# Kernel optimization log

Measured on AMD Instinct MI355X. Metric: run time of the kernel, lower is better.

Reference implementation:

```python
import jax, jax.numpy as jnp
import numpy as np

B, S, D, H = 2, 2048, 768, 12
HD = D // H
WINDOW = 64  # local_attention // 2
ROPE_THETA = 10000.0
NEG = -1e9


def setup_inputs() -> dict:
    key = jax.random.key(0)
    k1, k2, k3 = jax.random.split(key, 3)
    hidden_states = jax.random.normal(k1, (B, S, D), dtype=jnp.float32)
    Wqkv_w = jax.random.normal(k2, (3 * D, D), dtype=jnp.float32) * (D ** -0.5)
    Wo_w = jax.random.normal(k3, (D, D), dtype=jnp.float32) * (D ** -0.5)
    position_ids = jnp.broadcast_to(jnp.arange(S, dtype=jnp.int64 if jax.config.jax_enable_x64 else jnp.int32), (B, S))
    # additive sliding-window mask: 0 inside window, -1e9 outside (matches torch ModernBert mask construction)
    idx = np.arange(S)
    dist = np.abs(idx[:, None] - idx[None, :])
    sliding_window_mask = jnp.asarray(np.where(dist <= WINDOW, 0.0, NEG), dtype=jnp.float32)[None, None]  # [1,1,S,S]
    return {"hidden_states": hidden_states, "Wqkv_w": Wqkv_w, "Wo_w": Wo_w,
            "sliding_window_mask": sliding_window_mask, "position_ids": position_ids}


def _rotate_half(x):
    x1, x2 = jnp.split(x, 2, axis=-1)
    return jnp.concatenate([-x2, x1], axis=-1)


def reference(hidden_states, Wqkv_w, Wo_w, sliding_window_mask, position_ids):
    b, s, d = hidden_states.shape
    qkv = hidden_states @ Wqkv_w.T                      # [B,S,3D]
    qkv = qkv.reshape(b, s, 3, H, HD)
    q = qkv[:, :, 0].transpose(0, 2, 1, 3)              # [B,H,S,HD]
    k = qkv[:, :, 1].transpose(0, 2, 1, 3)
    v = qkv[:, :, 2].transpose(0, 2, 1, 3)
    # RoPE
    inv_freq = 1.0 / (ROPE_THETA ** (jnp.arange(0, HD, 2, dtype=jnp.float32) / HD))  # [HD/2]
    freqs = position_ids.astype(jnp.float32)[..., None] * inv_freq                   # [B,S,HD/2]
    emb = jnp.concatenate([freqs, freqs], axis=-1)                                   # [B,S,HD]
    cos = jnp.cos(emb)[:, None]                          # [B,1,S,HD]
    sin = jnp.sin(emb)[:, None]
    q = q * cos + _rotate_half(q) * sin
    k = k * cos + _rotate_half(k) * sin
    scale = HD ** -0.5
    scores = jnp.einsum('bhqd,bhkd->bhqk', q, k) * scale + sliding_window_mask       # [B,H,S,S]
    attn = jax.nn.softmax(scores.astype(jnp.float32), axis=-1).astype(q.dtype)
    out = jnp.einsum('bhqk,bhkd->bhqd', attn, v)         # [B,H,S,HD]
    out = out.transpose(0, 2, 1, 3).reshape(b, s, d)     # [B,S,D]
    return out @ Wo_w.T
```

## Files before the change

### kernel.cpp

```cpp
#include <hip/hip_runtime.h>
#include <hip/hip_bf16.h>
#include <cmath>

#define B_   2
#define S_   2048
#define D_   768
#define H_   12
#define HD_  64
#define WIN_ 64

typedef __bf16 bf16x8 __attribute__((ext_vector_type(8)));
typedef __bf16 bf16x4 __attribute__((ext_vector_type(4)));
typedef float  f32x4  __attribute__((ext_vector_type(4)));
typedef unsigned int u32;

__device__ __forceinline__ void async_ld16(const void* g, void* l) {
    __builtin_amdgcn_global_load_lds(
        (__attribute__((address_space(1))) void*)(size_t)g,
        (__attribute__((address_space(3))) void*)(u32)(size_t)l,
        16, 0, 0);
}

#define WAIT_VM0   0x0F70
#define WAIT_VM8   0x0F78
#define WAIT_LGKM0 0xC07F

#define NHS (B_ * S_ * D_)
#define NWQ (3 * D_ * D_)
#define NWO (D_ * D_)

__global__ __launch_bounds__(256) void to_bf16_3(const float* __restrict__ a,
                                                 const float* __restrict__ b,
                                                 const float* __restrict__ c,
                                                 __bf16* __restrict__ oa,
                                                 __bf16* __restrict__ ob,
                                                 __bf16* __restrict__ oc) {
    const int NA = NHS / 4, NB = NWQ / 4;
    int v = blockIdx.x * 256 + threadIdx.x;
    const float* src; __bf16* dst; int idx;
    if (v < NA)           { src = a; dst = oa; idx = v; }
    else if (v < NA + NB) { src = b; dst = ob; idx = v - NA; }
    else                  { src = c; dst = oc; idx = v - NA - NB; }
    float4 x = ((const float4*)src)[idx];
    bf16x4 y = { (__bf16)x.x, (__bf16)x.y, (__bf16)x.z, (__bf16)x.w };
    *(bf16x4*)(dst + (size_t)idx * 4) = y;
}

template <int MODE>
__global__ __launch_bounds__(128) void gemm_w(const __bf16* __restrict__ A,
                                              const __bf16* __restrict__ Bw,
                                              float* __restrict__ C,
                                              __bf16* __restrict__ qkv,
                                              __bf16* __restrict__ vt,
                                              const int* __restrict__ pos,
                                              int M, int N, int K) {
    __shared__ __attribute__((aligned(16))) char smem[2 * 16384];

    const int tid  = threadIdx.x;
    const int w    = tid >> 6;
    const int lane = tid & 63;
    const int id = blockIdx.x;
    const int m0 = (id & 63) << 6;
    const int n0 = (((id >> 6) << 1) + w) << 6;
    const int fr = lane & 15, fq = lane >> 4;
    const int sw = (fq + (fr >> 1)) & 3;

    __bf16* St = (__bf16*)(smem + w * 16384);

    f32x4 acc[4][4] = {};

    const int nkw = K >> 5;

    auto issue = [&](int ki, int buf) {
        const int k0 = ki << 5;
        __bf16* As = St + buf * 4096;
        __bf16* Bs = As + 2048;
        #pragma unroll
        for (int i = 0; i < 4; ++i) {
            const int c = i * 64 + lane;
            const int row = c >> 2, ccp = c & 3;
            const int cc = (ccp - (row >> 1)) & 3;
            async_ld16(A  + (size_t)(m0 + row) * K + k0 + cc * 8, As + c * 8);
            async_ld16(Bw + (size_t)(n0 + row) * K + k0 + cc * 8, Bs + c * 8);
        }
    };

    issue(0, 0);

    for (int ki = 0; ki < nkw; ++ki) {
        const int buf = ki & 1;
        if (ki + 1 < nkw) {
            __builtin_amdgcn_s_waitcnt(WAIT_LGKM0);
            issue(ki + 1, buf ^ 1);
            __builtin_amdgcn_s_waitcnt(WAIT_VM8);
        } else {
            __builtin_amdgcn_s_waitcnt(WAIT_VM0);
        }

        __bf16* As = St + buf * 4096;
        __bf16* Bs = As + 2048;
        bf16x8 af[4], bfv[4];
        #pragma unroll
        for (int t = 0; t < 4; ++t) {
            af[t]  = *(const bf16x8*)(As + (t * 16 + fr) * 32 + sw * 8);
            bfv[t] = *(const bf16x8*)(Bs + (t * 16 + fr) * 32 + sw * 8);
        }
        #pragma unroll
        for (int ti = 0; ti < 4; ++ti)
            #pragma unroll
            for (int tj = 0; tj < 4; ++tj)
                acc[ti][tj] = __builtin_amdgcn_mfma_f32_16x16x32_bf16(
                    af[ti], bfv[tj], acc[ti][tj], 0, 0, 0);
    }

    __builtin_amdgcn_s_waitcnt(WAIT_LGKM0);

    if (MODE == 0) {
        float* eL = (float*)St;
        #pragma unroll
        for (int half = 0; half < 2; ++half) {
            #pragma unroll
            for (int ti = 0; ti < 2; ++ti)
                #pragma unroll
                for (int tj = 0; tj < 4; ++tj)
                    #pragma unroll
                    for (int r = 0; r < 4; ++r)
                        eL[(ti * 16 + fq * 4 + r) * 65 + tj * 16 + fr] =
                            acc[half * 2 + ti][tj][r];
            #pragma unroll
            for (int p = 0; p < 8; ++p) {
                const int rc = p * 4 + (lane >> 4), ch = lane & 15;
                f32x4 vv = *(const f32x4*)(eL + rc * 65 + ch * 4);
                *(f32x4*)(C + (size_t)(m0 + half * 32 + rc) * N + n0 + ch * 4) = vv;
            }
        }
    } else if (n0 < 2 * D_) {
        const float invf0 = __powf(10000.0f, -(float)fr * (1.0f / 32.0f));
        const float invf1 = __powf(10000.0f, -(float)(16 + fr) * (1.0f / 32.0f));
        #pragma unroll
        for (int ti = 0; ti < 4; ++ti)
            #pragma unroll
            for (int r = 0; r < 4; ++r) {
                const int row = m0 + ti * 16 + fq * 4 + r;
                const float p = (float)pos[row];
                float s0, c0, s1, c1;
                __sincosf(p * invf0, &s0, &c0);
                __sincosf(p * invf1, &s1, &c1);
                const float x0 = acc[ti][0][r], x1 = acc[ti][2][r];
                acc[ti][0][r] = x0 * c0 - x1 * s0;
                acc[ti][2][r] = x1 * c0 + x0 * s0;
                const float y0 = acc[ti][1][r], y1 = acc[ti][3][r];
                acc[ti][1][r] = y0 * c1 - y1 * s1;
                acc[ti][3][r] = y1 * c1 + y0 * s1;
            }
        __bf16* eL = (__bf16*)St;
        #pragma unroll
        for (int ti = 0; ti < 4; ++ti)
            #pragma unroll
            for (int tj = 0; tj < 4; ++tj)
                #pragma unroll
                for (int r = 0; r < 4; ++r)
                    eL[(ti * 16 + fq * 4 + r) * 68 + tj * 16 + fr] = (__bf16)acc[ti][tj][r];
        #pragma unroll
        for (int p = 0; p < 8; ++p) {
            const int rq = p * 8 + (lane >> 3), ch = lane & 7;
            bf16x8 vv = *(const bf16x8*)(eL + rq * 68 + ch * 8);
            *(bf16x8*)(qkv + (size_t)(m0 + rq) * (2 * D_) + n0 + ch * 8) = vv;
        }
    } else {
        const int h = (n0 - 2 * D_) >> 6;
        const int bb = m0 >> 11, t0 = m0 & (S_ - 1);
        __bf16* eL = (__bf16*)St;
        #pragma unroll
        for (int ti = 0; ti < 4; ++ti)
            #pragma unroll
            for (int tj = 0; tj < 4; ++tj)
                #pragma unroll
                for (int r = 0; r < 4; ++r)
                    eL[(tj * 16 + fr) * 68 + ti * 16 + fq * 4 + r] = (__bf16)acc[ti][tj][r];
        const size_t vb = (size_t)((bb * H_ + h) * HD_) * S_ + t0;
        #pragma unroll
        for (int p = 0; p < 8; ++p) {
            const int d = p * 8 + (lane >> 3), ch = lane & 7;
            bf16x8 vv = *(const bf16x8*)(eL + d * 68 + ch * 8);
            *(bf16x8*)(vt + vb + (size_t)d * S_ + ch * 8) = vv;
        }
    }
}

__global__ __launch_bounds__(256) void attn_mfma(const __bf16* __restrict__ qkv,
                                                 const __bf16* __restrict__ vt,
                                                 __bf16* __restrict__ outb) {
    __shared__ __attribute__((aligned(16))) __bf16 smem[24576];
    __bf16* Ks  = smem;
    __bf16* Vts = smem + 12288;

    const int i0  = blockIdx.x * 64;
    const int h   = blockIdx.y;
    const int b   = blockIdx.z;
    const int tid = threadIdx.x;
    const int w = tid >> 6, lane = tid & 63;
    const int fr = lane & 15, fq = lane >> 4;
    const int wq0 = w * 16;

    #pragma unroll
    for (int i = 0; i < 6; ++i) {
        int c = i * 256 + tid;
        int ks = (i >= 3);
        int rem = c - ks * 768;
        int cc = rem & 3, row = rem >> 2;
        int j = i0 - 64 + row; j = min(max(j, 0), S_ - 1);
        async_ld16(qkv + ((size_t)b * S_ + j) * (2 * D_) + D_ + h * HD_ + ks * 32 + cc * 8,
                   Ks + c * 8);
    }
    const size_t vbase = (size_t)((b * H_ + h) * HD_) * S_;
    #pragma unroll
    for (int i = 0; i < 6; ++i) {
        int c = i * 256 + tid;
        int ks = c >> 8, rem = c & 255, d = rem >> 2, cc = rem & 3;
        int key = i0 - 64 + ks * 32 + cc * 8;
        key = min(max(key, 0), S_ - 8);
        async_ld16(vt + vbase + (size_t)d * S_ + key, Vts + c * 8);
    }

    const size_t qrow = ((size_t)b * S_ + i0 + wq0 + fr) * (2 * D_) + h * HD_;
    bf16x8 aq[2];
    aq[0] = *(const bf16x8*)(qkv + qrow + fq * 8);
    aq[1] = *(const bf16x8*)(qkv + qrow + 32 + fq * 8);

    __syncthreads();

    f32x4 sc[12] = {};
    #pragma unroll
    for (int nt = 0; nt < 12; ++nt) {
        #pragma unroll
        for (int ks = 0; ks < 2; ++ks) {
            bf16x8 bk = *(const bf16x8*)(Ks + (ks * 192 + nt * 16 + fr) * 32 + fq * 8);
            sc[nt] = __builtin_amdgcn_mfma_f32_16x16x32_bf16(aq[ks], bk, sc[nt], 0, 0, 0);
        }
    }

    float mx[4] = { -1e30f, -1e30f, -1e30f, -1e30f };
    #pragma unroll
    for (int nt = 0; nt < 12; ++nt) {
        const int jr = nt * 16 + fr;
        const int j  = i0 - 64 + jr;
        const bool jv = (j >= 0) && (j < S_);
        #pragma unroll
        for (int r = 0; r < 4; ++r) {
            const int ir = wq0 + fq * 4 + r + 64;
            const int dd = ir - jr;
            const bool v = jv && (dd <= WIN_) && (dd >= -WIN_);
            sc[nt][r] = v ? sc[nt][r] * 0.125f : -1e30f;
            mx[r] = fmaxf(mx[r], sc[nt][r]);
        }
    }
    #pragma unroll
    for (int r = 0; r < 4; ++r)
        #pragma unroll
        for (int off = 1; off < 16; off <<= 1)
            mx[r] = fmaxf(mx[r], __shfl_xor(mx[r], off, 64));

    float sm[4] = { 0.f, 0.f, 0.f, 0.f };
    #pragma unroll
    for (int nt = 0; nt < 12; ++nt)
        #pragma unroll
        for (int r = 0; r < 4; ++r) {
            float e = __expf(sc[nt][r] - mx[r]);
            sc[nt][r] = e;
            sm[r] += e;
        }
    #pragma unroll
    for (int r = 0; r < 4; ++r) {
        #pragma unroll
        for (int off = 1; off < 16; off <<= 1)
            sm[r] += __shfl_xor(sm[r], off, 64);
        sm[r] = 1.0f / sm[r];
    }

    __syncthreads();

    __bf16* Pw = Ks + w * 3072;
    #pragma unroll
    for (int nt = 0; nt < 12; ++nt) {
        const int ks = nt >> 1, kk = (nt & 1) * 16 + fr;
        #pragma unroll
        for (int r = 0; r < 4; ++r)
            Pw[(ks * 16 + fq * 4 + r) * 32 + kk] = (__bf16)(sc[nt][r] * sm[r]);
    }

    f32x4 oacc[4] = {};
    #pragma unroll
    for (int ks = 0; ks < 6; ++ks) {
        bf16x8 ap = *(const bf16x8*)(Pw + (ks * 16 + fr) * 32 + fq * 8);
        #pragma unroll
        for (int nt2 = 0; nt2 < 4; ++nt2) {
            bf16x8 bv = *(const bf16x8*)(Vts + (ks * 64 + nt2 * 16 + fr) * 32 + fq * 8);
            oacc[nt2] = __builtin_amdgcn_mfma_f32_16x16x32_bf16(ap, bv, oacc[nt2], 0, 0, 0);
        }
    }

    #pragma unroll
    for (int nt2 = 0; nt2 < 4; ++nt2)
        #pragma unroll
        for (int r = 0; r < 4; ++r)
            Pw[(fq * 4 + r) * 68 + nt2 * 16 + fr] = (__bf16)oacc[nt2][r];
    #pragma unroll
    for (int p = 0; p < 2; ++p) {
        const int q = p * 8 + (lane >> 3), ch = lane & 7;
        bf16x8 vv = *(const bf16x8*)(Pw + q * 68 + ch * 8);
        *(bf16x8*)(outb + ((size_t)b * S_ + i0 + wq0 + q) * D_ + h * HD_ + ch * 8) = vv;
    }
}

extern "C" void kernel_launch(void* const* d_in, const int* in_sizes, int n_in,
                              void* d_out, int out_size, void* d_ws, size_t ws_size,
                              hipStream_t stream) {
    const float* hs   = (const float*)d_in[0];
    const float* wqkv = (const float*)d_in[1];
    const float* wo   = (const float*)d_in[2];
    const int*   pos  = (const int*)d_in[4];
    float* out = (float*)d_out;

    __bf16* base    = (__bf16*)d_ws;
    __bf16* hs_bf   = base;
    __bf16* wqkv_bf = hs_bf + NHS;
    __bf16* wo_bf   = wqkv_bf + NWQ;
    __bf16* qkv     = wo_bf + NWO;
    __bf16* vt      = qkv + (size_t)(B_ * S_) * (2 * D_);
    __bf16* attn_bf = vt + (size_t)B_ * H_ * HD_ * S_;

    to_bf16_3<<<(NHS + NWQ + NWO) / 1024, 256, 0, stream>>>(
        hs, wqkv, wo, hs_bf, wqkv_bf, wo_bf);

    gemm_w<1><<<dim3(64 * (3 * D_ / 128)), 128, 0, stream>>>(
        hs_bf, wqkv_bf, nullptr, qkv, vt, pos, B_ * S_, 3 * D_, D_);

    attn_mfma<<<dim3(S_ / 64, H_, B_), 256, 0, stream>>>(qkv, vt, attn_bf);

    gemm_w<0><<<dim3(64 * (D_ / 128)), 128, 0, stream>>>(
        attn_bf, wo_bf, out, nullptr, nullptr, nullptr, B_ * S_, D_, D_);
}
```

Before: 146.9 us.

## Load GEMM fragments directly from global into registers with double buffering

Result: slower. 193.5 us (+31.8%).

```diff
diff --git a/kernel.cpp b/kernel.cpp
--- a/kernel.cpp
+++ b/kernel.cpp
@@ -20,10 +20,6 @@
         (__attribute__((address_space(3))) void*)(u32)(size_t)l,
         16, 0, 0);
 }
-
-#define WAIT_VM0   0x0F70
-#define WAIT_VM8   0x0F78
-#define WAIT_LGKM0 0xC07F
 
 #define NHS (B_ * S_ * D_)
 #define NWQ (3 * D_ * D_)
@@ -47,76 +43,61 @@
 }
 
 template <int MODE>
-__global__ __launch_bounds__(128) void gemm_w(const __bf16* __restrict__ A,
-                                              const __bf16* __restrict__ Bw,
-                                              float* __restrict__ C,
-                                              __bf16* __restrict__ qkv,
-                                              __bf16* __restrict__ vt,
-                                              const int* __restrict__ pos,
-                                              int M, int N, int K) {
-    __shared__ __attribute__((aligned(16))) char smem[2 * 16384];
+__global__ __launch_bounds__(256, 3) void gemm_r(const __bf16* __restrict__ A,
+                                                 const __bf16* __restrict__ Bw,
+                                                 float* __restrict__ C,
+                                                 __bf16* __restrict__ qkv,
+                                                 __bf16* __restrict__ vt,
+                                                 const int* __restrict__ pos,
+                                                 int M, int N, int K) {
+    __shared__ __attribute__((aligned(16))) char esmem[4][8704];
 
     const int tid  = threadIdx.x;
     const int w    = tid >> 6;
     const int lane = tid & 63;
     const int id = blockIdx.x;
     const int m0 = (id & 63) << 6;
-    const int n0 = (((id >> 6) << 1) + w) << 6;
+    const int n0 = (((id >> 6) << 2) + w) << 6;
     const int fr = lane & 15, fq = lane >> 4;
-    const int sw = (fq + (fr >> 1)) & 3;
-
-    __bf16* St = (__bf16*)(smem + w * 16384);
+
+    const __bf16* Ap = A  + (size_t)(m0 + fr) * K + fq * 8;
+    const __bf16* Bp = Bw + (size_t)(n0 + fr) * K + fq * 8;
+    const size_t rstep = (size_t)16 * K;
 
     f32x4 acc[4][4] = {};
-
-    const int nkw = K >> 5;
-
-    auto issue = [&](int ki, int buf) {
-        const int k0 = ki << 5;
-        __bf16* As = St + buf * 4096;
-        __bf16* Bs = As + 2048;
-        #pragma unroll
-        for (int i = 0; i < 4; ++i) {
-            const int c = i * 64 + lane;
-            const int row = c >> 2, ccp = c & 3;
-            const int cc = (ccp - (row >> 1)) & 3;
-            async_ld16(A  + (size_t)(m0 + row) * K + k0 + cc * 8, As + c * 8);
-            async_ld16(Bw + (size_t)(n0 + row) * K + k0 + cc * 8, Bs + c * 8);
+    bf16x8 a0[4], b0[4], a1[4], b1[4];
+
+    auto LD = [&](bf16x8 (&ar)[4], bf16x8 (&br)[4], int kk) {
+        const int ko = kk << 5;
+        #pragma unroll
+        for (int t = 0; t < 4; ++t) {
+            ar[t] = *(const bf16x8*)(Ap + (size_t)t * rstep + ko);
+            br[t] = *(const bf16x8*)(Bp + (size_t)t * rstep + ko);
         }
     };
-
-    issue(0, 0);
-
-    for (int ki = 0; ki < nkw; ++ki) {
-        const int buf = ki & 1;
-        if (ki + 1 < nkw) {
-            __builtin_amdgcn_s_waitcnt(WAIT_LGKM0);
-            issue(ki + 1, buf ^ 1);
-            __builtin_amdgcn_s_waitcnt(WAIT_VM8);
-        } else {
-            __builtin_amdgcn_s_waitcnt(WAIT_VM0);
-        }
-
-        __bf16* As = St + buf * 4096;
-        __bf16* Bs = As + 2048;
-        bf16x8 af[4], bfv[4];
-        #pragma unroll
-        for (int t = 0; t < 4; ++t) {
-            af[t]  = *(const bf16x8*)(As + (t * 16 + fr) * 32 + sw * 8);
-            bfv[t] = *(const bf16x8*)(Bs + (t * 16 + fr) * 32 + sw * 8);
-        }
+    auto MM = [&](const bf16x8 (&ar)[4], const bf16x8 (&br)[4]) {
         #pragma unroll
         for (int ti = 0; ti < 4; ++ti)
             #pragma unroll
             for (int tj = 0; tj < 4; ++tj)
                 acc[ti][tj] = __builtin_amdgcn_mfma_f32_16x16x32_bf16(
-                    af[ti], bfv[tj], acc[ti][tj], 0, 0, 0);
-    }
-
-    __builtin_amdgcn_s_waitcnt(WAIT_LGKM0);
+                    ar[ti], br[tj], acc[ti][tj], 0, 0, 0);
+    };
+
+    const int nkw = K >> 5;
+    LD(a0, b0, 0);
+    for (int kk = 0; kk + 2 < nkw; kk += 2) {
+        LD(a1, b1, kk + 1);
+        MM(a0, b0);
+        LD(a0, b0, kk + 2);
+        MM(a1, b1);
+    }
+    LD(a1, b1, nkw - 1);
+    MM(a0, b0);
+    MM(a1, b1);
 
     if (MODE == 0) {
-        float* eL = (float*)St;
+        float* eL = (float*)esmem[w];
         #pragma unroll
         for (int half = 0; half < 2; ++half) {
             #pragma unroll
@@ -153,7 +134,7 @@
                 acc[ti][1][r] = y0 * c1 - y1 * s1;
                 acc[ti][3][r] = y1 * c1 + y0 * s1;
             }
-        __bf16* eL = (__bf16*)St;
+        __bf16* eL = (__bf16*)esmem[w];
         #pragma unroll
         for (int ti = 0; ti < 4; ++ti)
             #pragma unroll
@@ -170,7 +151,7 @@
     } else {
         const int h = (n0 - 2 * D_) >> 6;
         const int bb = m0 >> 11, t0 = m0 & (S_ - 1);
-        __bf16* eL = (__bf16*)St;
+        __bf16* eL = (__bf16*)esmem[w];
         #pragma unroll
         for (int ti = 0; ti < 4; ++ti)
             #pragma unroll
@@ -333,11 +314,11 @@
     to_bf16_3<<<(NHS + NWQ + NWO) / 1024, 256, 0, stream>>>(
         hs, wqkv, wo, hs_bf, wqkv_bf, wo_bf);
 
-    gemm_w<1><<<dim3(64 * (3 * D_ / 128)), 128, 0, stream>>>(
+    gemm_r<1><<<dim3(64 * (3 * D_ / 256)), 256, 0, stream>>>(
         hs_bf, wqkv_bf, nullptr, qkv, vt, pos, B_ * S_, 3 * D_, D_);
 
     attn_mfma<<<dim3(S_ / 64, H_, B_), 256, 0, stream>>>(qkv, vt, attn_bf);
 
-    gemm_w<0><<<dim3(64 * (D_ / 128)), 128, 0, stream>>>(
+    gemm_r<0><<<dim3(64 * (D_ / 256)), 256, 0, stream>>>(
         attn_bf, wo_bf, out, nullptr, nullptr, nullptr, B_ * S_, D_, D_);
 }
```
